# Performance work log

Measured on AMD Instinct MI355X. Metric: run time of the kernel, lower is better.

## Reference

```python
import jax, jax.numpy as jnp
import numpy as np


def _apply_ry(state, angle, wire):
    # state: (B, P, 2,2,2,2) real statevector; angle: scalar or (B, P)
    ax = 2 + wire
    st = jnp.moveaxis(state, ax, -1)
    c = jnp.cos(angle * 0.5)
    s = jnp.sin(angle * 0.5)
    extra = st.ndim - 1 - jnp.ndim(c)
    c = jnp.reshape(c, jnp.shape(c) + (1,) * extra)
    s = jnp.reshape(s, jnp.shape(s) + (1,) * extra)
    s0, s1 = st[..., 0], st[..., 1]
    out = jnp.stack([c * s0 - s * s1, s * s0 + c * s1], axis=-1)
    return jnp.moveaxis(out, -1, ax)


def _apply_cnot(state, control, target):
    st = jnp.moveaxis(state, (2 + control, 2 + target), (-2, -1))
    out = jnp.stack([st[..., 0, :], st[..., 1, ::-1]], axis=-2)
    return jnp.moveaxis(out, (-2, -1), (2 + control, 2 + target))


def _run_circuit(patch_vals, params):
    # patch_vals: (B, P, 4) angles; params: (L, 4). All gates (RY, CNOT) are real,
    # so the statevector stays real float32. Simulates all B*P circuits at once.
    B, P, _ = patch_vals.shape
    state = jnp.zeros((B, P, 2, 2, 2, 2), patch_vals.dtype).at[:, :, 0, 0, 0, 0].set(1.0)
    for w in range(4):
        state = _apply_ry(state, patch_vals[:, :, w], w)
    for l in range(params.shape[0]):
        state = _apply_ry(state, params[l, 0], 0)
        state = _apply_ry(state, params[l, 1], 1)
        state = _apply_cnot(state, 0, 1)
        state = _apply_ry(state, params[l, 2], 2)
        state = _apply_ry(state, params[l, 3], 3)
        state = _apply_cnot(state, 2, 3)
    prob = state * state
    # <Z_w> = P(bit_w = 0) - P(bit_w = 1)
    z = [(jnp.take(prob, 0, axis=2 + w) - jnp.take(prob, 1, axis=2 + w)).sum(axis=(2, 3, 4))
         for w in range(4)]
    return jnp.stack(z, axis=-1)  # (B, P, 4)


def _forward(x, params, W, b):
    B = x.shape[0]
    xi = x[:, 0]  # (B, 28, 28)
    # torch Unfold(2, stride=2): per-patch order (kh, kw); patches row-major -> (B, 196, 4)
    p2 = xi.reshape(B, 14, 2, 14, 2).transpose(0, 1, 3, 2, 4).reshape(B, 196, 4)
    qfeat = _run_circuit(p2, params).reshape(B, 196 * 4)  # (B, 784), patch-major
    # torch Unfold(4, stride=4) gives (B, 16, 49); .view(B, -1) -> (kernel_pos, patch) order
    cfeat = xi.reshape(B, 7, 4, 7, 4).transpose(0, 2, 4, 1, 3).reshape(B, 16 * 49)
    feats = jnp.concatenate([qfeat, cfeat], axis=1)  # (B, 1568)
    logits = feats @ W.T + b
    return jax.nn.log_softmax(logits, axis=-1)


def setup_inputs():
    key = jax.random.key(0)
    k1, k2, k3 = jax.random.split(key, 3)
    B = 2048
    x = jax.random.normal(k1, (B, 1, 28, 28), dtype=jnp.float32)
    params = jax.random.normal(k2, (4, 4), dtype=jnp.float32)
    W = jax.random.normal(k3, (10, 1568), dtype=jnp.float32) * 0.05
    b = jnp.zeros((10,), dtype=jnp.float32)
    return {"x": x, "params": params, "W": W, "b": b}


def reference(x, params, W, b):
    return _forward(x, params, W, b)
```

## Files before the change

kernel.cpp:

```cpp
#include <hip/hip_runtime.h>
#include <math.h>

#define TPB 512

typedef __fp16 half2v __attribute__((ext_vector_type(2)));
typedef __fp16 half4v __attribute__((ext_vector_type(4)));
typedef __fp16 half8v __attribute__((ext_vector_type(8)));

template <int CTRL, int RMASK>
__device__ inline float dpp_add(float v) {
    int t = __builtin_amdgcn_update_dpp(0, __float_as_int(v), CTRL, RMASK, 0xf, false);
    return v + __int_as_float(t);
}
__device__ inline float wave_sum_bcast(float v) {
    v = dpp_add<0x111, 0xf>(v);
    v = dpp_add<0x112, 0xf>(v);
    v = dpp_add<0x114, 0xf>(v);
    v = dpp_add<0x118, 0xf>(v);
    v = dpp_add<0x142, 0xa>(v);
    v = dpp_add<0x143, 0xc>(v);
    return __int_as_float(__builtin_amdgcn_readlane(__float_as_int(v), 63));
}

#if __has_builtin(__builtin_amdgcn_fdot2)
#define HAVE_FDOT2 1
#else
#define HAVE_FDOT2 0
#endif

__global__ __launch_bounds__(TPB) void quanv_one_kernel(
    const float* __restrict__ x,
    const float* __restrict__ params,
    const float* __restrict__ W,
    const float* __restrict__ bias,
    float* __restrict__ out,
    int B, int L)
{
    __shared__ __align__(16) __fp16 wlds[15680];
    __shared__ __align__(16) float umat[32];

    const int tid  = threadIdx.x;
    const int lane = tid & 63;
    const int wv   = tid >> 6;

    for (int g = tid; g < 3920; g += TPB) {
        if (g < 1960) {
            int e  = g * 4;
            int c  = e / 784;
            int q0 = e - c * 784;
            float4 q = *(const float4*)(W + c * 1568 + q0);
            half4v o;
            o[0] = (__fp16)q.x; o[1] = (__fp16)q.y;
            o[2] = (__fp16)q.z; o[3] = (__fp16)q.w;
            *(half4v*)(wlds + (c * 196 + (q0 >> 2)) * 8) = o;
        } else {
            int e   = (g - 1960) * 4;
            int c   = e / 784;
            int cf0 = e - c * 784;
            float4 q = *(const float4*)(W + c * 1568 + 784 + cf0);
            float qv[4] = {q.x, q.y, q.z, q.w};
#pragma unroll
            for (int d = 0; d < 4; ++d) {
                int cf = cf0 + d;
                int a  = cf / 196;
                int r1 = cf - a * 196;
                int bb = r1 / 49;
                int r2 = r1 - bb * 49;
                int i  = r2 / 7;
                int j  = r2 - i * 7;
                int t  = 28 * i + 7 * a + j;
                wlds[(c * 196 + t) * 8 + 4 + bb] = (__fp16)qv[d];
            }
        }
    }

    if (tid < 2) {
        const int f = tid;
        float M[16];
#pragma unroll
        for (int i = 0; i < 16; ++i) M[i] = (i % 5 == 0) ? 1.f : 0.f;
        for (int l = 0; l < L; ++l) {
            float A = params[4 * l + 2 * f + 0] * 0.5f;
            float C = __cosf(A), S = __sinf(A);
#pragma unroll
            for (int q = 0; q < 4; ++q) {
                float a0 = M[q],     a2 = M[8 + q];
                M[q]      = C * a0 - S * a2;  M[8 + q]  = S * a0 + C * a2;
                float a1 = M[4 + q], a3 = M[12 + q];
                M[4 + q]  = C * a1 - S * a3;  M[12 + q] = S * a1 + C * a3;
            }
            A = params[4 * l + 2 * f + 1] * 0.5f;
            C = __cosf(A); S = __sinf(A);
#pragma unroll
            for (int q = 0; q < 4; ++q) {
                float a0 = M[q],     a1 = M[4 + q];
                M[q]      = C * a0 - S * a1;  M[4 + q]  = S * a0 + C * a1;
                float a2 = M[8 + q], a3 = M[12 + q];
                M[8 + q]  = C * a2 - S * a3;  M[12 + q] = S * a2 + C * a3;
            }
#pragma unroll
            for (int q = 0; q < 4; ++q) {
                float tm = M[8 + q]; M[8 + q] = M[12 + q]; M[12 + q] = tm;
            }
        }
#pragma unroll
        for (int i = 0; i < 16; ++i) umat[f * 16 + i] = M[i];
    }

    __syncthreads();

    const int img = blockIdx.x * 8 + wv;
    if (img >= B) return;

    float Um[32];
#pragma unroll
    for (int j = 0; j < 8; ++j) ((float4*)Um)[j] = ((const float4*)umat)[j];

    const float* xb = x + (size_t)img * 784;

    float acc[10];
#pragma unroll
    for (int c = 0; c < 10; ++c) acc[c] = 0.f;

#pragma unroll
    for (int r = 0; r < 4; ++r) {
        int t = r * 64 + lane;
        if (t < 196) {
            int pi = t / 14, pj = t - pi * 14;
            float2 top = *(const float2*)(xb + 56 * pi + 2 * pj);
            float2 bot = *(const float2*)(xb + 56 * pi + 2 * pj + 28);
            float4 cim = *(const float4*)(xb + 4 * t);

            float c0 = __cosf(0.5f * top.x), s0 = __sinf(0.5f * top.x);
            float c1 = __cosf(0.5f * top.y), s1 = __sinf(0.5f * top.y);
            float c2 = __cosf(0.5f * bot.x), s2 = __sinf(0.5f * bot.x);
            float c3 = __cosf(0.5f * bot.y), s3 = __sinf(0.5f * bot.y);

            float ui0 = c0 * c1, ui1 = c0 * s1, ui2 = s0 * c1, ui3 = s0 * s1;
            float vi0 = c2 * c3, vi1 = c2 * s3, vi2 = s2 * c3, vi3 = s2 * s3;

            float uf0 = fmaf(Um[0],  ui0, fmaf(Um[1],  ui1, fmaf(Um[2],  ui2, Um[3]  * ui3)));
            float uf1 = fmaf(Um[4],  ui0, fmaf(Um[5],  ui1, fmaf(Um[6],  ui2, Um[7]  * ui3)));
            float uf2 = fmaf(Um[8],  ui0, fmaf(Um[9],  ui1, fmaf(Um[10], ui2, Um[11] * ui3)));
            float uf3 = fmaf(Um[12], ui0, fmaf(Um[13], ui1, fmaf(Um[14], ui2, Um[15] * ui3)));
            float vf0 = fmaf(Um[16], vi0, fmaf(Um[17], vi1, fmaf(Um[18], vi2, Um[19] * vi3)));
            float vf1 = fmaf(Um[20], vi0, fmaf(Um[21], vi1, fmaf(Um[22], vi2, Um[23] * vi3)));
            float vf2 = fmaf(Um[24], vi0, fmaf(Um[25], vi1, fmaf(Um[26], vi2, Um[27] * vi3)));
            float vf3 = fmaf(Um[28], vi0, fmaf(Um[29], vi1, fmaf(Um[30], vi2, Um[31] * vi3)));

            float p0 = uf0 * uf0, p1 = uf1 * uf1, p2 = uf2 * uf2, p3 = uf3 * uf3;
            float q0 = vf0 * vf0, q1 = vf1 * vf1, q2 = vf2 * vf2, q3 = vf3 * vf3;
            float z0 = (p0 + p1) - (p2 + p3);
            float z1 = (p0 + p2) - (p1 + p3);
            float z2 = (q0 + q1) - (q2 + q3);
            float z3 = (q0 + q2) - (q1 + q3);

            half2v f0 = __builtin_amdgcn_cvt_pkrtz(z0, z1);
            half2v f1 = __builtin_amdgcn_cvt_pkrtz(z2, z3);
            half2v f2 = __builtin_amdgcn_cvt_pkrtz(cim.x, cim.y);
            half2v f3 = __builtin_amdgcn_cvt_pkrtz(cim.z, cim.w);

#pragma unroll
            for (int c = 0; c < 10; ++c) {
                half8v w = *(const half8v*)(wlds + (c * 196 + t) * 8);
                half2v w0 = __builtin_shufflevector(w, w, 0, 1);
                half2v w1 = __builtin_shufflevector(w, w, 2, 3);
                half2v w2 = __builtin_shufflevector(w, w, 4, 5);
                half2v w3 = __builtin_shufflevector(w, w, 6, 7);
                float a = acc[c];
#if HAVE_FDOT2
                a = __builtin_amdgcn_fdot2(f0, w0, a, false);
                a = __builtin_amdgcn_fdot2(f1, w1, a, false);
                a = __builtin_amdgcn_fdot2(f2, w2, a, false);
                a = __builtin_amdgcn_fdot2(f3, w3, a, false);
#else
                a = fmaf((float)f0[0], (float)w0[0], a);
                a = fmaf((float)f0[1], (float)w0[1], a);
                a = fmaf((float)f1[0], (float)w1[0], a);
                a = fmaf((float)f1[1], (float)w1[1], a);
                a = fmaf((float)f2[0], (float)w2[0], a);
                a = fmaf((float)f2[1], (float)w2[1], a);
                a = fmaf((float)f3[0], (float)w3[0], a);
                a = fmaf((float)f3[1], (float)w3[1], a);
#endif
                acc[c] = a;
            }
        }
    }

    float l0 = wave_sum_bcast(acc[0]) + bias[0];
    float l1 = wave_sum_bcast(acc[1]) + bias[1];
    float l2 = wave_sum_bcast(acc[2]) + bias[2];
    float l3 = wave_sum_bcast(acc[3]) + bias[3];
    float l4 = wave_sum_bcast(acc[4]) + bias[4];
    float l5 = wave_sum_bcast(acc[5]) + bias[5];
    float l6 = wave_sum_bcast(acc[6]) + bias[6];
    float l7 = wave_sum_bcast(acc[7]) + bias[7];
    float l8 = wave_sum_bcast(acc[8]) + bias[8];
    float l9 = wave_sum_bcast(acc[9]) + bias[9];

    float m = fmaxf(fmaxf(fmaxf(fmaxf(l0, l1), fmaxf(l2, l3)),
                          fmaxf(fmaxf(l4, l5), fmaxf(l6, l7))),
                    fmaxf(l8, l9));
    float se = __expf(l0 - m) + __expf(l1 - m) + __expf(l2 - m) + __expf(l3 - m) +
               __expf(l4 - m) + __expf(l5 - m) + __expf(l6 - m) + __expf(l7 - m) +
               __expf(l8 - m) + __expf(l9 - m);
    float lse = __logf(se) + m;

    if (lane < 10) {
        float o = l0 - lse;
        o = (lane == 1) ? l1 - lse : o;
        o = (lane == 2) ? l2 - lse : o;
        o = (lane == 3) ? l3 - lse : o;
        o = (lane == 4) ? l4 - lse : o;
        o = (lane == 5) ? l5 - lse : o;
        o = (lane == 6) ? l6 - lse : o;
        o = (lane == 7) ? l7 - lse : o;
        o = (lane == 8) ? l8 - lse : o;
        o = (lane == 9) ? l9 - lse : o;
        out[(size_t)img * 10 + lane] = o;
    }
}

extern "C" void kernel_launch(void* const* d_in, const int* in_sizes, int n_in,
                              void* d_out, int out_size, void* d_ws, size_t ws_size,
                              hipStream_t stream) {
    const float* x      = (const float*)d_in[0];
    const float* params = (const float*)d_in[1];
    const float* W      = (const float*)d_in[2];
    const float* bias   = (const float*)d_in[3];
    float* out          = (float*)d_out;

    const int B = in_sizes[0] / 784;
    const int L = in_sizes[1] / 4;

    const int nblk = (B + 7) / 8;
    quanv_one_kernel<<<dim3(nblk), dim3(TPB), 0, stream>>>(x, params, W, bias, out, B, L);
}
```

Before: 12.89 us.

## Process two images per wave to reuse LDS weight loads

Each wavefront now handles two images instead of one, so every fp16 weight vector read from LDS feeds two dot-product accumulations. The block size drops to 256 threads while still covering 8 images per block, which halves the per-block cost of staging W into LDS and building the unitary. All global loads for both images are issued up front to overlap memory latency. In exchange, register pressure roughly doubles, there are half as many waves per block, and launch_bounds(TPB,1) lets the compiler use more registers, which may lower occupancy.

New measurement: 16.18 us. +25.5%, slower.

```diff
diff --git a/kernel.cpp b/kernel.cpp
--- a/kernel.cpp
+++ b/kernel.cpp
@@ -1,7 +1,7 @@
 #include <hip/hip_runtime.h>
 #include <math.h>
 
-#define TPB 512
+#define TPB 256
 
 typedef __fp16 half2v __attribute__((ext_vector_type(2)));
 typedef __fp16 half4v __attribute__((ext_vector_type(4)));
@@ -28,7 +28,7 @@
 #define HAVE_FDOT2 0
 #endif
 
-__global__ __launch_bounds__(TPB) void quanv_one_kernel(
+__global__ __launch_bounds__(TPB, 1) void quanv_one_kernel(
     const float* __restrict__ x,
     const float* __restrict__ params,
     const float* __restrict__ W,
@@ -109,36 +109,46 @@
 
     __syncthreads();
 
-    const int img = blockIdx.x * 8 + wv;
-    if (img >= B) return;
+    const int img0 = blockIdx.x * 8 + wv * 2;
+    const int img1 = img0 + 1;
+    const float* xa = x + (size_t)((img0 < B) ? img0 : (B - 1)) * 784;
+    const float* xb = x + (size_t)((img1 < B) ? img1 : (B - 1)) * 784;
 
     float Um[32];
 #pragma unroll
     for (int j = 0; j < 8; ++j) ((float4*)Um)[j] = ((const float4*)umat)[j];
 
-    const float* xb = x + (size_t)img * 784;
-
-    float acc[10];
-#pragma unroll
-    for (int c = 0; c < 10; ++c) acc[c] = 0.f;
-
+    float2 topA[4], botA[4], topB[4], botB[4];
+    float4 cimA[4], cimB[4];
 #pragma unroll
     for (int r = 0; r < 4; ++r) {
         int t = r * 64 + lane;
         if (t < 196) {
             int pi = t / 14, pj = t - pi * 14;
-            float2 top = *(const float2*)(xb + 56 * pi + 2 * pj);
-            float2 bot = *(const float2*)(xb + 56 * pi + 2 * pj + 28);
-            float4 cim = *(const float4*)(xb + 4 * t);
-
-            float c0 = __cosf(0.5f * top.x), s0 = __sinf(0.5f * top.x);
-            float c1 = __cosf(0.5f * top.y), s1 = __sinf(0.5f * top.y);
-            float c2 = __cosf(0.5f * bot.x), s2 = __sinf(0.5f * bot.x);
-            float c3 = __cosf(0.5f * bot.y), s3 = __sinf(0.5f * bot.y);
-
+            int po = 56 * pi + 2 * pj;
+            topA[r] = *(const float2*)(xa + po);
+            botA[r] = *(const float2*)(xa + po + 28);
+            cimA[r] = *(const float4*)(xa + 4 * t);
+            topB[r] = *(const float2*)(xb + po);
+            botB[r] = *(const float2*)(xb + po + 28);
+            cimB[r] = *(const float4*)(xb + 4 * t);
+        }
+    }
+
+    float accA[10], accB[10];
+#pragma unroll
+    for (int c = 0; c < 10; ++c) { accA[c] = 0.f; accB[c] = 0.f; }
+
+#pragma unroll
+    for (int r = 0; r < 4; ++r) {
+        int t = r * 64 + lane;
+        if (t < 196) {
+            float c0 = __cosf(0.5f * topA[r].x), s0 = __sinf(0.5f * topA[r].x);
+            float c1 = __cosf(0.5f * topA[r].y), s1 = __sinf(0.5f * topA[r].y);
+            float c2 = __cosf(0.5f * botA[r].x), s2 = __sinf(0.5f * botA[r].x);
+            float c3 = __cosf(0.5f * botA[r].y), s3 = __sinf(0.5f * botA[r].y);
             float ui0 = c0 * c1, ui1 = c0 * s1, ui2 = s0 * c1, ui3 = s0 * s1;
             float vi0 = c2 * c3, vi1 = c2 * s3, vi2 = s2 * c3, vi3 = s2 * s3;
-
             float uf0 = fmaf(Um[0],  ui0, fmaf(Um[1],  ui1, fmaf(Um[2],  ui2, Um[3]  * ui3)));
             float uf1 = fmaf(Um[4],  ui0, fmaf(Um[5],  ui1, fmaf(Um[6],  ui2, Um[7]  * ui3)));
             float uf2 = fmaf(Um[8],  ui0, fmaf(Um[9],  ui1, fmaf(Um[10], ui2, Um[11] * ui3)));
@@ -147,18 +157,33 @@
             float vf1 = fmaf(Um[20], vi0, fmaf(Um[21], vi1, fmaf(Um[22], vi2, Um[23] * vi3)));
             float vf2 = fmaf(Um[24], vi0, fmaf(Um[25], vi1, fmaf(Um[26], vi2, Um[27] * vi3)));
             float vf3 = fmaf(Um[28], vi0, fmaf(Um[29], vi1, fmaf(Um[30], vi2, Um[31] * vi3)));
-
             float p0 = uf0 * uf0, p1 = uf1 * uf1, p2 = uf2 * uf2, p3 = uf3 * uf3;
             float q0 = vf0 * vf0, q1 = vf1 * vf1, q2 = vf2 * vf2, q3 = vf3 * vf3;
-            float z0 = (p0 + p1) - (p2 + p3);
-            float z1 = (p0 + p2) - (p1 + p3);
-            float z2 = (q0 + q1) - (q2 + q3);
-            float z3 = (q0 + q2) - (q1 + q3);
-
-            half2v f0 = __builtin_amdgcn_cvt_pkrtz(z0, z1);
-            half2v f1 = __builtin_amdgcn_cvt_pkrtz(z2, z3);
-            half2v f2 = __builtin_amdgcn_cvt_pkrtz(cim.x, cim.y);
-            half2v f3 = __builtin_amdgcn_cvt_pkrtz(cim.z, cim.w);
+            half2v fa0 = __builtin_amdgcn_cvt_pkrtz((p0 + p1) - (p2 + p3), (p0 + p2) - (p1 + p3));
+            half2v fa1 = __builtin_amdgcn_cvt_pkrtz((q0 + q1) - (q2 + q3), (q0 + q2) - (q1 + q3));
+            half2v fa2 = __builtin_amdgcn_cvt_pkrtz(cimA[r].x, cimA[r].y);
+            half2v fa3 = __builtin_amdgcn_cvt_pkrtz(cimA[r].z, cimA[r].w);
+
+            c0 = __cosf(0.5f * topB[r].x); s0 = __sinf(0.5f * topB[r].x);
+            c1 = __cosf(0.5f * topB[r].y); s1 = __sinf(0.5f * topB[r].y);
+            c2 = __cosf(0.5f * botB[r].x); s2 = __sinf(0.5f * botB[r].x);
+            c3 = __cosf(0.5f * botB[r].y); s3 = __sinf(0.5f * botB[r].y);
+            ui0 = c0 * c1; ui1 = c0 * s1; ui2 = s0 * c1; ui3 = s0 * s1;
+            vi0 = c2 * c3; vi1 = c2 * s3; vi2 = s2 * c3; vi3 = s2 * s3;
+            uf0 = fmaf(Um[0],  ui0, fmaf(Um[1],  ui1, fmaf(Um[2],  ui2, Um[3]  * ui3)));
+            uf1 = fmaf(Um[4],  ui0, fmaf(Um[5],  ui1, fmaf(Um[6],  ui2, Um[7]  * ui3)));
+            uf2 = fmaf(Um[8],  ui0, fmaf(Um[9],  ui1, fmaf(Um[10], ui2, Um[11] * ui3)));
+            uf3 = fmaf(Um[12], ui0, fmaf(Um[13], ui1, fmaf(Um[14], ui2, Um[15] * ui3)));
+            vf0 = fmaf(Um[16], vi0, fmaf(Um[17], vi1, fmaf(Um[18], vi2, Um[19] * vi3)));
+            vf1 = fmaf(Um[20], vi0, fmaf(Um[21], vi1, fmaf(Um[22], vi2, Um[23] * vi3)));
+            vf2 = fmaf(Um[24], vi0, fmaf(Um[25], vi1, fmaf(Um[26], vi2, Um[27] * vi3)));
+            vf3 = fmaf(Um[28], vi0, fmaf(Um[29], vi1, fmaf(Um[30], vi2, Um[31] * vi3)));
+            p0 = uf0 * uf0; p1 = uf1 * uf1; p2 = uf2 * uf2; p3 = uf3 * uf3;
+            q0 = vf0 * vf0; q1 = vf1 * vf1; q2 = vf2 * vf2; q3 = vf3 * vf3;
+            half2v fb0 = __builtin_amdgcn_cvt_pkrtz((p0 + p1) - (p2 + p3), (p0 + p2) - (p1 + p3));
+            half2v fb1 = __builtin_amdgcn_cvt_pkrtz((q0 + q1) - (q2 + q3), (q0 + q2) - (q1 + q3));
+            half2v fb2 = __builtin_amdgcn_cvt_pkrtz(cimB[r].x, cimB[r].y);
+            half2v fb3 = __builtin_amdgcn_cvt_pkrtz(cimB[r].z, cimB[r].w);
 
 #pragma unroll
             for (int c = 0; c < 10; ++c) {
@@ -167,58 +192,86 @@
                 half2v w1 = __builtin_shufflevector(w, w, 2, 3);
                 half2v w2 = __builtin_shufflevector(w, w, 4, 5);
                 half2v w3 = __builtin_shufflevector(w, w, 6, 7);
-                float a = acc[c];
 #if HAVE_FDOT2
-                a = __builtin_amdgcn_fdot2(f0, w0, a, false);
-                a = __builtin_amdgcn_fdot2(f1, w1, a, false);
-                a = __builtin_amdgcn_fdot2(f2, w2, a, false);
-                a = __builtin_amdgcn_fdot2(f3, w3, a, false);
+                float a = accA[c];
+                a = __builtin_amdgcn_fdot2(fa0, w0, a, false);
+                a = __builtin_amdgcn_fdot2(fa1, w1, a, false);
+                a = __builtin_amdgcn_fdot2(fa2, w2, a, false);
+                a = __builtin_amdgcn_fdot2(fa3, w3, a, false);
+                accA[c] = a;
+                float b = accB[c];
+                b = __builtin_amdgcn_fdot2(fb0, w0, b, false);
+                b = __builtin_amdgcn_fdot2(fb1, w1, b, false);
+                b = __builtin_amdgcn_fdot2(fb2, w2, b, false);
+                b = __builtin_amdgcn_fdot2(fb3, w3, b, false);
+                accB[c] = b;
 #else
-                a = fmaf((float)f0[0], (float)w0[0], a);
-                a = fmaf((float)f0[1], (float)w0[1], a);
-                a = fmaf((float)f1[0], (float)w1[0], a);
-                a = fmaf((float)f1[1], (float)w1[1], a);
-                a = fmaf((float)f2[0], (float)w2[0], a);
-                a = fmaf((float)f2[1], (float)w2[1], a);
-                a = fmaf((float)f3[0], (float)w3[0], a);
-                a = fmaf((float)f3[1], (float)w3[1], a);
+                float a = accA[c];
+                a = fmaf((float)fa0[0], (float)w0[0], a); a = fmaf((float)fa0[1], (float)w0[1], a);
+                a = fmaf((float)fa1[0], (float)w1[0], a); a = fmaf((float)fa1[1], (float)w1[1], a);
+                a = fmaf((float)fa2[0], (float)w2[0], a); a = fmaf((float)fa2[1], (float)w2[1], a);
+                a = fmaf((float)fa3[0], (float)w3[0], a); a = fmaf((float)fa3[1], (float)w3[1], a);
+                accA[c] = a;
+                float b = accB[c];
+                b = fmaf((float)fb0[0], (float)w0[0], b); b = fmaf((float)fb0[1], (float)w0[1], b);
+                b = fmaf((float)fb1[0], (float)w1[0], b); b = fmaf((float)fb1[1], (float)w1[1], b);
+                b = fmaf((float)fb2[0], (float)w2[0], b); b = fmaf((float)fb2[1], (float)w2[1], b);
+                b = fmaf((float)fb3[0], (float)w3[0], b); b = fmaf((float)fb3[1], (float)w3[1], b);
+                accB[c] = b;
 #endif
-                acc[c] = a;
-            }
-        }
-    }
-
-    float l0 = wave_sum_bcast(acc[0]) + bias[0];
-    float l1 = wave_sum_bcast(acc[1]) + bias[1];
-    float l2 = wave_sum_bcast(acc[2]) + bias[2];
-    float l3 = wave_sum_bcast(acc[3]) + bias[3];
-    float l4 = wave_sum_bcast(acc[4]) + bias[4];
-    float l5 = wave_sum_bcast(acc[5]) + bias[5];
-    float l6 = wave_sum_bcast(acc[6]) + bias[6];
-    float l7 = wave_sum_bcast(acc[7]) + bias[7];
-    float l8 = wave_sum_bcast(acc[8]) + bias[8];
-    float l9 = wave_sum_bcast(acc[9]) + bias[9];
-
-    float m = fmaxf(fmaxf(fmaxf(fmaxf(l0, l1), fmaxf(l2, l3)),
-                          fmaxf(fmaxf(l4, l5), fmaxf(l6, l7))),
-                    fmaxf(l8, l9));
-    float se = __expf(l0 - m) + __expf(l1 - m) + __expf(l2 - m) + __expf(l3 - m) +
-               __expf(l4 - m) + __expf(l5 - m) + __expf(l6 - m) + __expf(l7 - m) +
-               __expf(l8 - m) + __expf(l9 - m);
-    float lse = __logf(se) + m;
-
-    if (lane < 10) {
-        float o = l0 - lse;
-        o = (lane == 1) ? l1 - lse : o;
-        o = (lane == 2) ? l2 - lse : o;
-        o = (lane == 3) ? l3 - lse : o;
-        o = (lane == 4) ? l4 - lse : o;
-        o = (lane == 5) ? l5 - lse : o;
-        o = (lane == 6) ? l6 - lse : o;
-        o = (lane == 7) ? l7 - lse : o;
-        o = (lane == 8) ? l8 - lse : o;
-        o = (lane == 9) ? l9 - lse : o;
-        out[(size_t)img * 10 + lane] = o;
+            }
+        }
+    }
+
+    float lgA[10], lgB[10];
+#pragma unroll
+    for (int c = 0; c < 10; ++c) lgA[c] = wave_sum_bcast(accA[c]) + bias[c];
+#pragma unroll
+    for (int c = 0; c < 10; ++c) lgB[c] = wave_sum_bcast(accB[c]) + bias[c];
+
+    if (img0 < B) {
+        float m = lgA[0];
+#pragma unroll
+        for (int c = 1; c < 10; ++c) m = fmaxf(m, lgA[c]);
+        float se = 0.f;
+#pragma unroll
+        for (int c = 0; c < 10; ++c) se += __expf(lgA[c] - m);
+        float lse = __logf(se) + m;
+        if (lane < 10) {
+            float o = lgA[0];
+            o = (lane == 1) ? lgA[1] : o;
+            o = (lane == 2) ? lgA[2] : o;
+            o = (lane == 3) ? lgA[3] : o;
+            o = (lane == 4) ? lgA[4] : o;
+            o = (lane == 5) ? lgA[5] : o;
+            o = (lane == 6) ? lgA[6] : o;
+            o = (lane == 7) ? lgA[7] : o;
+            o = (lane == 8) ? lgA[8] : o;
+            o = (lane == 9) ? lgA[9] : o;
+            out[(size_t)img0 * 10 + lane] = o - lse;
+        }
+    }
+    if (img1 < B) {
+        float m = lgB[0];
+#pragma unroll
+        for (int c = 1; c < 10; ++c) m = fmaxf(m, lgB[c]);
+        float se = 0.f;
+#pragma unroll
+        for (int c = 0; c < 10; ++c) se += __expf(lgB[c] - m);
+        float lse = __logf(se) + m;
+        if (lane < 10) {
+            float o = lgB[0];
+            o = (lane == 1) ? lgB[1] : o;
+            o = (lane == 2) ? lgB[2] : o;
+            o = (lane == 3) ? lgB[3] : o;
+            o = (lane == 4) ? lgB[4] : o;
+            o = (lane == 5) ? lgB[5] : o;
+            o = (lane == 6) ? lgB[6] : o;
+            o = (lane == 7) ? lgB[7] : o;
+            o = (lane == 8) ? lgB[8] : o;
+            o = (lane == 9) ? lgB[9] : o;
+            out[(size_t)img1 * 10 + lane] = o - lse;
+        }
     }
 }
 
```
